# Kernel tuning notes

Measured on AMD Instinct MI355X. Metric: run time of the kernel, lower is better.

Reference implementation:

```python
import jax, jax.numpy as jnp
import numpy as np

EMB = 256  # embedding_dim


def setup_inputs() -> dict:
    key = jax.random.key(0)
    k1, k2, k3 = jax.random.split(key, 3)
    B, P, N, D = 32, 4, 1024, EMB
    x = jax.random.normal(k1, (B, P, N, D), dtype=jnp.float32)
    W_qkv = jax.random.normal(k2, (D, 1 + 2 * D), dtype=jnp.float32) * (1.0 / np.sqrt(D))
    b_qkv = jnp.zeros((1 + 2 * D,), dtype=jnp.float32)
    W_o = jax.random.normal(k3, (D, D), dtype=jnp.float32) * (1.0 / np.sqrt(D))
    b_o = jnp.zeros((D,), dtype=jnp.float32)
    return {"x": x, "W_qkv": W_qkv, "b_qkv": b_qkv, "W_o": W_o, "b_o": b_o}


def reference(x, W_qkv, b_qkv, W_o, b_o):
    # x: [B, P, N, D]
    D = W_o.shape[0]
    qkv = jnp.einsum('bpnd,de->bpne', x, W_qkv) + b_qkv  # [B,P,N,1+2D]
    q = qkv[..., :1]                 # [B,P,N,1]
    k = qkv[..., 1:1 + D]            # [B,P,N,D]
    v = jax.nn.relu(qkv[..., 1 + D:])  # [B,P,N,D]
    # softmax over the patch axis N (axis=2)
    context_scores = jax.nn.softmax(q, axis=2)  # [B,P,N,1]
    # dropout layers operate in inference mode here (identity)
    context_vector = jnp.sum(k * context_scores, axis=2, keepdims=True)  # [B,P,1,D]
    updated_values = v * context_vector  # broadcast multiply, [B,P,N,D]
    final = jnp.einsum('bpnd,de->bpne', updated_values, W_o) + b_o  # [B,P,N,D]
    return final
```

## Files before the change

kernel.cpp:

```cpp
#include <hip/hip_runtime.h>


typedef float  floatx4 __attribute__((ext_vector_type(4)));
typedef __bf16 bf16x8  __attribute__((ext_vector_type(8)));
typedef unsigned short u16;
typedef u16 u16x8 __attribute__((ext_vector_type(8)));

#define NGRP 128

__device__ __forceinline__ float bf2f(u16 u) {
    union { unsigned int i; float f; } c; c.i = ((unsigned int)u) << 16; return c.f;
}
__device__ __forceinline__ u16 f2bf(float f) {
    union { __bf16 h; u16 u; } c; c.h = (__bf16)f; return c.u;
}
__device__ __forceinline__ floatx4 mfma16(bf16x8 a, bf16x8 b, floatx4 c) {
    return __builtin_amdgcn_mfma_f32_16x16x32_bf16(a, b, c, 0, 0, 0);
}

__global__ __launch_bounds__(256) void k_zero(float* __restrict__ cvu,
                                              float* __restrict__ Sg) {
    const int i = blockIdx.x * 256 + threadIdx.x;
    if (i < NGRP * 256) cvu[i] = 0.f;
    if (i < NGRP) Sg[i] = 0.f;
}

__global__ __launch_bounds__(256) void k_repack(
    const float* __restrict__ Wqkv, const float* __restrict__ Wo,
    u16* __restrict__ Wqkv_p, u16* __restrict__ Wo_p)
{
    const int i = blockIdx.x * 256 + threadIdx.x;
    if (i < 33 * 4096) {
        const int j = i & 7, lane = (i >> 3) & 63, kk = (i >> 9) & 7, ct = i >> 12;
        const int k = kk * 32 + (lane >> 4) * 8 + j;
        const int n16 = lane & 15;
        float v;
        if (ct < 32) v = Wqkv[k * 513 + (1 + ct * 16 + n16)];
        else         v = (n16 == 0) ? Wqkv[k * 513] : 0.f;
        Wqkv_p[i] = f2bf(v);
    }
    if (i < 16 * 4096) {
        const int j = i & 7, lane = (i >> 3) & 63, kk = (i >> 9) & 7, ct = i >> 12;
        const int k = kk * 32 + (lane >> 4) * 8 + j;
        const int n = ct * 16 + (lane & 15);
        Wo_p[i] = f2bf(Wo[k * 256 + n]);
    }
}

__global__ __launch_bounds__(256, 2) void k_qkv(
    const float* __restrict__ x, const u16* __restrict__ Wp,
    const float* __restrict__ bqkv, u16* __restrict__ Vw,
    float* __restrict__ cvu, float* __restrict__ Sg)
{
    const int tid = threadIdx.x;
    const int w = tid >> 6, lane = tid & 63, quad = lane >> 4, n16 = lane & 15;
    const int m0 = blockIdx.x * 64;
    const int g  = blockIdx.x >> 4;

    __shared__ u16 As[64 * 256];
    __shared__ float e_s[64];

#pragma unroll
    for (int i = 0; i < 8; i++) {
        const int c = i * 256 + tid;
        const int row = c >> 5, col = c & 31;
        const float* xp = x + (size_t)(m0 + row) * 256 + col * 8;
        floatx4 u0 = *(const floatx4*)xp;
        floatx4 u1 = *(const floatx4*)(xp + 4);
        u16x8 o;
        o[0] = f2bf(u0[0]); o[1] = f2bf(u0[1]); o[2] = f2bf(u0[2]); o[3] = f2bf(u0[3]);
        o[4] = f2bf(u1[0]); o[5] = f2bf(u1[1]); o[6] = f2bf(u1[2]); o[7] = f2bf(u1[3]);
        *(u16x8*)(As + row * 256 + ((col ^ (row & 15)) * 8)) = o;
    }
    __syncthreads();

    floatx4 acc[8][4];
    floatx4 accq[4];
#pragma unroll
    for (int i = 0; i < 8; i++)
#pragma unroll
        for (int rt = 0; rt < 4; rt++) acc[i][rt] = (floatx4){0.f, 0.f, 0.f, 0.f};
#pragma unroll
    for (int rt = 0; rt < 4; rt++) accq[rt] = (floatx4){0.f, 0.f, 0.f, 0.f};

#pragma unroll
    for (int kk = 0; kk < 8; kk++) {
        bf16x8 a[4];
#pragma unroll
        for (int rt = 0; rt < 4; rt++) {
            const int row = rt * 16 + n16;
            a[rt] = __builtin_bit_cast(bf16x8,
                *(const u16x8*)(As + row * 256 + (((kk * 4 + quad) ^ n16) * 8)));
        }
#pragma unroll
        for (int i = 0; i < 8; i++) {
            const int ct = w + 4 * i;
            bf16x8 b = __builtin_bit_cast(bf16x8,
                *(const u16x8*)(Wp + (size_t)((ct * 8 + kk) * 64 + lane) * 8));
#pragma unroll
            for (int rt = 0; rt < 4; rt++) acc[i][rt] = mfma16(a[rt], b, acc[i][rt]);
        }
        if (w == 0) {
            bf16x8 b = __builtin_bit_cast(bf16x8,
                *(const u16x8*)(Wp + (size_t)((32 * 8 + kk) * 64 + lane) * 8));
#pragma unroll
            for (int rt = 0; rt < 4; rt++) accq[rt] = mfma16(a[rt], b, accq[rt]);
        }
    }

    if (w == 0 && n16 == 0) {
        const float bq = bqkv[0];
#pragma unroll
        for (int rt = 0; rt < 4; rt++)
#pragma unroll
            for (int r = 0; r < 4; r++)
                e_s[rt * 16 + quad * 4 + r] = __expf(accq[rt][r] + bq);
    }
    __syncthreads();

    if (tid < 64) {
        float e = e_s[tid];
#pragma unroll
        for (int s = 32; s > 0; s >>= 1) e += __shfl_xor(e, s, 64);
        if (tid == 0) atomicAdd(Sg + g, e);
    }

    float ev[16];
#pragma unroll
    for (int rt = 0; rt < 4; rt++)
#pragma unroll
        for (int r = 0; r < 4; r++) ev[rt * 4 + r] = e_s[rt * 16 + quad * 4 + r];

#pragma unroll
    for (int i = 0; i < 4; i++) {
        const int c = (w + 4 * i) * 16 + n16;
        const float bias = bqkv[1 + c];
        float p = 0.f;
#pragma unroll
        for (int rt = 0; rt < 4; rt++)
#pragma unroll
            for (int r = 0; r < 4; r++) p += ev[rt * 4 + r] * (acc[i][rt][r] + bias);
        p += __shfl_xor(p, 16, 64);
        p += __shfl_xor(p, 32, 64);
        if (lane < 16) atomicAdd(cvu + g * 256 + c, p);
    }

#pragma unroll
    for (int i = 4; i < 8; i++) {
        const int cfull = (w + 4 * i) * 16 + n16;
        const float bias = bqkv[1 + cfull];
        const int cvn = cfull - 256;
#pragma unroll
        for (int rt = 0; rt < 4; rt++) {
            const int rowb = m0 + rt * 16 + quad * 4;
#pragma unroll
            for (int r = 0; r < 4; r++)
                Vw[(size_t)(rowb + r) * 256 + cvn] = f2bf(fmaxf(acc[i][rt][r] + bias, 0.f));
        }
    }
}

__global__ __launch_bounds__(256, 2) void k_out(
    const u16* __restrict__ Vw, const u16* __restrict__ Wop,
    const float* __restrict__ cvu, const float* __restrict__ Sg,
    const float* __restrict__ bo, float* __restrict__ out)
{
    const int tid = threadIdx.x;
    const int w = tid >> 6, lane = tid & 63, quad = lane >> 4, n16 = lane & 15;
    const int m0 = blockIdx.x * 64;
    const int g  = blockIdx.x >> 4;

    __shared__ u16 Vs[64 * 256];
    __shared__ float cvs[256];

    cvs[tid] = cvu[g * 256 + tid] * (1.0f / Sg[g]);

#pragma unroll
    for (int i = 0; i < 8; i++) {
        const int c = i * 256 + tid;
        const int row = c >> 5, col = c & 31;
        u16x8 v = *(const u16x8*)(Vw + (size_t)(m0 + row) * 256 + col * 8);
        *(u16x8*)(Vs + row * 256 + ((col ^ (row & 15)) * 8)) = v;
    }
    __syncthreads();

    floatx4 acc[4][4];
#pragma unroll
    for (int i = 0; i < 4; i++)
#pragma unroll
        for (int rt = 0; rt < 4; rt++) acc[i][rt] = (floatx4){0.f, 0.f, 0.f, 0.f};

#pragma unroll
    for (int kk = 0; kk < 8; kk++) {
        bf16x8 a[4];
#pragma unroll
        for (int rt = 0; rt < 4; rt++) {
            const int row = rt * 16 + n16;
            a[rt] = __builtin_bit_cast(bf16x8,
                *(const u16x8*)(Vs + row * 256 + (((kk * 4 + quad) ^ n16) * 8)));
        }
        const floatx4 c0 = *(const floatx4*)(cvs + kk * 32 + quad * 8);
        const floatx4 c1 = *(const floatx4*)(cvs + kk * 32 + quad * 8 + 4);
#pragma unroll
        for (int i = 0; i < 4; i++) {
            const int ct = w + 4 * i;
            u16x8 wo = *(const u16x8*)(Wop + (size_t)((ct * 8 + kk) * 64 + lane) * 8);
            bf16x8 b;
            b[0] = (__bf16)(c0[0] * bf2f(wo[0]));
            b[1] = (__bf16)(c0[1] * bf2f(wo[1]));
            b[2] = (__bf16)(c0[2] * bf2f(wo[2]));
            b[3] = (__bf16)(c0[3] * bf2f(wo[3]));
            b[4] = (__bf16)(c1[0] * bf2f(wo[4]));
            b[5] = (__bf16)(c1[1] * bf2f(wo[5]));
            b[6] = (__bf16)(c1[2] * bf2f(wo[6]));
            b[7] = (__bf16)(c1[3] * bf2f(wo[7]));
#pragma unroll
            for (int rt = 0; rt < 4; rt++) acc[i][rt] = mfma16(a[rt], b, acc[i][rt]);
        }
    }

#pragma unroll
    for (int i = 0; i < 4; i++) {
        const int c = (w + 4 * i) * 16 + n16;
        const float bias = bo[c];
#pragma unroll
        for (int rt = 0; rt < 4; rt++) {
            const int rowb = m0 + rt * 16 + quad * 4;
#pragma unroll
            for (int r = 0; r < 4; r++)
                out[(size_t)(rowb + r) * 256 + c] = acc[i][rt][r] + bias;
        }
    }
}

extern "C" void kernel_launch(void* const* d_in, const int* in_sizes, int n_in,
                              void* d_out, int out_size, void* d_ws, size_t ws_size,
                              hipStream_t stream)
{
    const float* x    = (const float*)d_in[0];
    const float* Wqkv = (const float*)d_in[1];
    const float* bqkv = (const float*)d_in[2];
    const float* Wo   = (const float*)d_in[3];
    const float* bo   = (const float*)d_in[4];
    float* out = (float*)d_out;

    char* ws = (char*)d_ws;
    u16*   Vw    = (u16*)(ws);
    u16*   Wqkvp = (u16*)(ws + 67108864);
    u16*   Wop   = (u16*)(ws + 67379200);
    float* cvu   = (float*)(ws + 67510272);
    float* Sg    = (float*)(ws + 67641344);

    k_zero  <<<129, 256, 0, stream>>>(cvu, Sg);
    k_repack<<<528, 256, 0, stream>>>(Wqkv, Wo, Wqkvp, Wop);
    k_qkv   <<<2048, 256, 0, stream>>>(x, Wqkvp, bqkv, Vw, cvu, Sg);
    k_out   <<<2048, 256, 0, stream>>>(Vw, Wop, cvu, Sg, bo, out);
}
```

Baseline: 344.8 us.

## Use 512-thread blocks, compute q via scalar dot, merge prep kernels

Doubles the workgroup size of both main kernels to 512 threads (8 waves), so each wave handles half as many output column tiles and carries fewer accumulator registers, with launch bounds requesting more resident blocks. The single-column q projection leaves the padded MFMA tile and becomes an fp32 dot product against x in LDS, computed before the main GEMM, which removes the extra masked MFMA work done only by wave 0. The zero-fill and weight-repack kernels are merged into a single prep kernel to save one launch. The cost is an extra barrier and a small LDS reduction pass before the MFMA loop, and each wave now has less independent MFMA work in flight.

```diff
diff --git a/kernel.cpp b/kernel.cpp
--- a/kernel.cpp
+++ b/kernel.cpp
@@ -18,39 +18,31 @@
     return __builtin_amdgcn_mfma_f32_16x16x32_bf16(a, b, c, 0, 0, 0);
 }
 
-__global__ __launch_bounds__(256) void k_zero(float* __restrict__ cvu,
-                                              float* __restrict__ Sg) {
+__global__ __launch_bounds__(256) void k_prep(
+    const float* __restrict__ Wqkv, const float* __restrict__ Wo,
+    u16* __restrict__ Wqkv_p, u16* __restrict__ Wo_p,
+    float* __restrict__ wqp, float* __restrict__ cvu, float* __restrict__ Sg)
+{
     const int i = blockIdx.x * 256 + threadIdx.x;
-    if (i < NGRP * 256) cvu[i] = 0.f;
-    if (i < NGRP) Sg[i] = 0.f;
-}
-
-__global__ __launch_bounds__(256) void k_repack(
-    const float* __restrict__ Wqkv, const float* __restrict__ Wo,
-    u16* __restrict__ Wqkv_p, u16* __restrict__ Wo_p)
-{
-    const int i = blockIdx.x * 256 + threadIdx.x;
-    if (i < 33 * 4096) {
+    if (i < 32 * 4096) {
         const int j = i & 7, lane = (i >> 3) & 63, kk = (i >> 9) & 7, ct = i >> 12;
         const int k = kk * 32 + (lane >> 4) * 8 + j;
-        const int n16 = lane & 15;
-        float v;
-        if (ct < 32) v = Wqkv[k * 513 + (1 + ct * 16 + n16)];
-        else         v = (n16 == 0) ? Wqkv[k * 513] : 0.f;
-        Wqkv_p[i] = f2bf(v);
+        Wqkv_p[i] = f2bf(Wqkv[k * 513 + (1 + ct * 16 + (lane & 15))]);
     }
     if (i < 16 * 4096) {
         const int j = i & 7, lane = (i >> 3) & 63, kk = (i >> 9) & 7, ct = i >> 12;
         const int k = kk * 32 + (lane >> 4) * 8 + j;
-        const int n = ct * 16 + (lane & 15);
-        Wo_p[i] = f2bf(Wo[k * 256 + n]);
-    }
-}
-
-__global__ __launch_bounds__(256, 2) void k_qkv(
+        Wo_p[i] = f2bf(Wo[k * 256 + (ct * 16 + (lane & 15))]);
+    }
+    if (i < 256) wqp[i] = Wqkv[i * 513];
+    if (i < NGRP * 256) cvu[i] = 0.f;
+    if (i < NGRP) Sg[i] = 0.f;
+}
+
+__global__ __launch_bounds__(512, 4) void k_qkv(
     const float* __restrict__ x, const u16* __restrict__ Wp,
-    const float* __restrict__ bqkv, u16* __restrict__ Vw,
-    float* __restrict__ cvu, float* __restrict__ Sg)
+    const float* __restrict__ wqp, const float* __restrict__ bqkv,
+    u16* __restrict__ Vw, float* __restrict__ cvu, float* __restrict__ Sg)
 {
     const int tid = threadIdx.x;
     const int w = tid >> 6, lane = tid & 63, quad = lane >> 4, n16 = lane & 15;
@@ -61,8 +53,8 @@
     __shared__ float e_s[64];
 
 #pragma unroll
-    for (int i = 0; i < 8; i++) {
-        const int c = i * 256 + tid;
+    for (int it = 0; it < 4; it++) {
+        const int c = it * 512 + tid;
         const int row = c >> 5, col = c & 31;
         const float* xp = x + (size_t)(m0 + row) * 256 + col * 8;
         floatx4 u0 = *(const floatx4*)xp;
@@ -74,14 +66,32 @@
     }
     __syncthreads();
 
-    floatx4 acc[8][4];
-    floatx4 accq[4];
-#pragma unroll
-    for (int i = 0; i < 8; i++)
+    {
+        const int r = tid >> 3, s = tid & 7;
+        float qacc = 0.f;
+#pragma unroll
+        for (int j = 0; j < 4; j++) {
+            const int c = s * 4 + j;
+            u16x8 xv = *(const u16x8*)(As + r * 256 + ((c ^ (r & 15)) * 8));
+            floatx4 w0 = *(const floatx4*)(wqp + c * 8);
+            floatx4 w1 = *(const floatx4*)(wqp + c * 8 + 4);
+            qacc += bf2f(xv[0]) * w0[0] + bf2f(xv[1]) * w0[1]
+                  + bf2f(xv[2]) * w0[2] + bf2f(xv[3]) * w0[3]
+                  + bf2f(xv[4]) * w1[0] + bf2f(xv[5]) * w1[1]
+                  + bf2f(xv[6]) * w1[2] + bf2f(xv[7]) * w1[3];
+        }
+        qacc += __shfl_xor(qacc, 1, 64);
+        qacc += __shfl_xor(qacc, 2, 64);
+        qacc += __shfl_xor(qacc, 4, 64);
+        if (s == 0) e_s[r] = __expf(qacc + bqkv[0]);
+    }
+    __syncthreads();
+
+    floatx4 acc[4][4];
+#pragma unroll
+    for (int i = 0; i < 4; i++)
 #pragma unroll
         for (int rt = 0; rt < 4; rt++) acc[i][rt] = (floatx4){0.f, 0.f, 0.f, 0.f};
-#pragma unroll
-    for (int rt = 0; rt < 4; rt++) accq[rt] = (floatx4){0.f, 0.f, 0.f, 0.f};
 
 #pragma unroll
     for (int kk = 0; kk < 8; kk++) {
@@ -93,30 +103,14 @@
                 *(const u16x8*)(As + row * 256 + (((kk * 4 + quad) ^ n16) * 8)));
         }
 #pragma unroll
-        for (int i = 0; i < 8; i++) {
-            const int ct = w + 4 * i;
+        for (int i = 0; i < 4; i++) {
+            const int ct = w + 8 * i;
             bf16x8 b = __builtin_bit_cast(bf16x8,
                 *(const u16x8*)(Wp + (size_t)((ct * 8 + kk) * 64 + lane) * 8));
 #pragma unroll
             for (int rt = 0; rt < 4; rt++) acc[i][rt] = mfma16(a[rt], b, acc[i][rt]);
         }
-        if (w == 0) {
-            bf16x8 b = __builtin_bit_cast(bf16x8,
-                *(const u16x8*)(Wp + (size_t)((32 * 8 + kk) * 64 + lane) * 8));
-#pragma unroll
-            for (int rt = 0; rt < 4; rt++) accq[rt] = mfma16(a[rt], b, accq[rt]);
-        }
-    }
-
-    if (w == 0 && n16 == 0) {
-        const float bq = bqkv[0];
-#pragma unroll
-        for (int rt = 0; rt < 4; rt++)
-#pragma unroll
-            for (int r = 0; r < 4; r++)
-                e_s[rt * 16 + quad * 4 + r] = __expf(accq[rt][r] + bq);
-    }
-    __syncthreads();
+    }
 
     if (tid < 64) {
         float e = e_s[tid];
@@ -125,29 +119,24 @@
         if (tid == 0) atomicAdd(Sg + g, e);
     }
 
-    float ev[16];
-#pragma unroll
-    for (int rt = 0; rt < 4; rt++)
-#pragma unroll
-        for (int r = 0; r < 4; r++) ev[rt * 4 + r] = e_s[rt * 16 + quad * 4 + r];
-
-#pragma unroll
-    for (int i = 0; i < 4; i++) {
-        const int c = (w + 4 * i) * 16 + n16;
+#pragma unroll
+    for (int i = 0; i < 2; i++) {
+        const int c = (w + 8 * i) * 16 + n16;
         const float bias = bqkv[1 + c];
         float p = 0.f;
 #pragma unroll
         for (int rt = 0; rt < 4; rt++)
 #pragma unroll
-            for (int r = 0; r < 4; r++) p += ev[rt * 4 + r] * (acc[i][rt][r] + bias);
+            for (int r = 0; r < 4; r++)
+                p += e_s[rt * 16 + quad * 4 + r] * (acc[i][rt][r] + bias);
         p += __shfl_xor(p, 16, 64);
         p += __shfl_xor(p, 32, 64);
         if (lane < 16) atomicAdd(cvu + g * 256 + c, p);
     }
 
 #pragma unroll
-    for (int i = 4; i < 8; i++) {
-        const int cfull = (w + 4 * i) * 16 + n16;
+    for (int i = 2; i < 4; i++) {
+        const int cfull = (w + 8 * i) * 16 + n16;
         const float bias = bqkv[1 + cfull];
         const int cvn = cfull - 256;
 #pragma unroll
@@ -160,7 +149,7 @@
     }
 }
 
-__global__ __launch_bounds__(256, 2) void k_out(
+__global__ __launch_bounds__(512, 4) void k_out(
     const u16* __restrict__ Vw, const u16* __restrict__ Wop,
     const float* __restrict__ cvu, const float* __restrict__ Sg,
     const float* __restrict__ bo, float* __restrict__ out)
@@ -173,20 +162,20 @@
     __shared__ u16 Vs[64 * 256];
     __shared__ float cvs[256];
 
-    cvs[tid] = cvu[g * 256 + tid] * (1.0f / Sg[g]);
-
-#pragma unroll
-    for (int i = 0; i < 8; i++) {
-        const int c = i * 256 + tid;
+    if (tid < 256) cvs[tid] = cvu[g * 256 + tid] * (1.0f / Sg[g]);
+
+#pragma unroll
+    for (int it = 0; it < 4; it++) {
+        const int c = it * 512 + tid;
         const int row = c >> 5, col = c & 31;
         u16x8 v = *(const u16x8*)(Vw + (size_t)(m0 + row) * 256 + col * 8);
         *(u16x8*)(Vs + row * 256 + ((col ^ (row & 15)) * 8)) = v;
     }
     __syncthreads();
 
-    floatx4 acc[4][4];
-#pragma unroll
-    for (int i = 0; i < 4; i++)
+    floatx4 acc[2][4];
+#pragma unroll
+    for (int i = 0; i < 2; i++)
 #pragma unroll
         for (int rt = 0; rt < 4; rt++) acc[i][rt] = (floatx4){0.f, 0.f, 0.f, 0.f};
 
@@ -202,8 +191,8 @@
         const floatx4 c0 = *(const floatx4*)(cvs + kk * 32 + quad * 8);
         const floatx4 c1 = *(const floatx4*)(cvs + kk * 32 + quad * 8 + 4);
 #pragma unroll
-        for (int i = 0; i < 4; i++) {
-            const int ct = w + 4 * i;
+        for (int i = 0; i < 2; i++) {
+            const int ct = w + 8 * i;
             u16x8 wo = *(const u16x8*)(Wop + (size_t)((ct * 8 + kk) * 64 + lane) * 8);
             bf16x8 b;
             b[0] = (__bf16)(c0[0] * bf2f(wo[0]));
@@ -220,8 +209,8 @@
     }
 
 #pragma unroll
-    for (int i = 0; i < 4; i++) {
-        const int c = (w + 4 * i) * 16 + n16;
+    for (int i = 0; i < 2; i++) {
+        const int c = (w + 8 * i) * 16 + n16;
         const float bias = bo[c];
 #pragma unroll
         for (int rt = 0; rt < 4; rt++) {
@@ -247,12 +236,12 @@
     char* ws = (char*)d_ws;
     u16*   Vw    = (u16*)(ws);
     u16*   Wqkvp = (u16*)(ws + 67108864);
-    u16*   Wop   = (u16*)(ws + 67379200);
-    float* cvu   = (float*)(ws + 67510272);
-    float* Sg    = (float*)(ws + 67641344);
-
-    k_zero  <<<129, 256, 0, stream>>>(cvu, Sg);
-    k_repack<<<528, 256, 0, stream>>>(Wqkv, Wo, Wqkvp, Wop);
-    k_qkv   <<<2048, 256, 0, stream>>>(x, Wqkvp, bqkv, Vw, cvu, Sg);
-    k_out   <<<2048, 256, 0, stream>>>(Vw, Wop, cvu, Sg, bo, out);
-}
+    u16*   Wop   = (u16*)(ws + 67371008);
+    float* wqp   = (float*)(ws + 67502080);
+    float* cvu   = (float*)(ws + 67503104);
+    float* Sg    = (float*)(ws + 67634176);
+
+    k_prep<<<512, 256, 0, stream>>>(Wqkv, Wo, Wqkvp, Wop, wqp, cvu, Sg);
+    k_qkv <<<2048, 512, 0, stream>>>(x, Wqkvp, wqp, bqkv, Vw, cvu, Sg);
+    k_out <<<2048, 512, 0, stream>>>(Vw, Wop, cvu, Sg, bo, out);
+}
```

Result: faster. 309.2 us (-10.3%).
